# Kernel optimization log

Hardware: AMD Instinct MI355X
Metric: run time of the kernel (lower is better)

## Reference

```python
import jax, jax.numpy as jnp
import numpy as np

NUM_EMBEDDINGS = 512
EMBEDDING_DIM = 256
COMMITMENT_COST = 0.25


def setup_inputs() -> dict:
    key = jax.random.key(0)
    k1, k2 = jax.random.split(key)
    z_e = jax.random.normal(k1, (16, EMBEDDING_DIM, 16, 16, 16), dtype=jnp.float32)
    # codebook init: uniform(-1/K, 1/K) as in the torch module
    codebook = jax.random.uniform(
        k2, (NUM_EMBEDDINGS, EMBEDDING_DIM), dtype=jnp.float32,
        minval=-1.0 / NUM_EMBEDDINGS, maxval=1.0 / NUM_EMBEDDINGS)
    return {"z_e": z_e, "codebook": codebook}


def reference(z_e, codebook):
    # z_e: [B, C, D, H, W] -> [B, D, H, W, C]
    z_p = jnp.transpose(z_e, (0, 2, 3, 4, 1))
    spatial_shape = z_p.shape[:-1]
    flat = z_p.reshape(-1, EMBEDDING_DIM)                      # [N, C]
    z_sq = jnp.sum(flat * flat, axis=1, keepdims=True)         # [N, 1]
    cb_sq = jnp.sum(codebook * codebook, axis=1)[None, :]      # [1, K]
    dot = flat @ codebook.T                                    # [N, K]
    distances = z_sq + cb_sq - 2.0 * dot
    idx = jnp.argmin(distances, axis=1)                        # [N]
    z_q_p = codebook[idx].reshape(z_p.shape)                   # [B, D, H, W, C]
    codebook_loss = jnp.mean((z_q_p - jax.lax.stop_gradient(z_p)) ** 2)
    commitment_loss = jnp.mean((z_p - jax.lax.stop_gradient(z_q_p)) ** 2)
    vq_loss = codebook_loss + COMMITMENT_COST * commitment_loss
    # straight-through estimator
    z_q_st = z_p + jax.lax.stop_gradient(z_q_p - z_p)
    z_q = jnp.transpose(z_q_st, (0, 4, 1, 2, 3))               # [B, C, D, H, W]
    encoding_indices = idx.reshape(spatial_shape)
    return z_q, vq_loss, encoding_indices
```

## Files before the change

kernel.cpp:

```cpp
#include <hip/hip_runtime.h>

#define NPOS   65536
#define CDIM   256
#define KCODES 512
#define ZTOT   16777216
#define IDX_OFF (ZTOT + 1)
#define TAU    2.0e-3f
#define GL_CAP 16384

#define WS_CBSQ 64
#define WS_CBBF 66112
#define WS_GLI  132096
#define NC_FULL 0x7fff

using bf16x8 = __attribute__((ext_vector_type(8))) short;
using f32x4  = __attribute__((ext_vector_type(4))) float;

__device__ __forceinline__ unsigned short f2bf(float f) {
    unsigned int u = __float_as_uint(f);
    return (unsigned short)((u + 0x7fffu + ((u >> 16) & 1u)) >> 16);
}

__device__ __forceinline__ float np_pw128_sq(const float* a) {
    float r[8];
    #pragma unroll
    for (int j = 0; j < 8; ++j) r[j] = __fmul_rn(a[j], a[j]);
    #pragma unroll 1
    for (int i = 8; i < 128; i += 8) {
        #pragma unroll
        for (int j = 0; j < 8; ++j)
            r[j] = __fadd_rn(r[j], __fmul_rn(a[i + j], a[i + j]));
    }
    return __fadd_rn(__fadd_rn(__fadd_rn(r[0], r[1]), __fadd_rn(r[2], r[3])),
                     __fadd_rn(__fadd_rn(r[4], r[5]), __fadd_rn(r[6], r[7])));
}

__global__ void vq_cvtprep(const float* __restrict__ cb, float* __restrict__ ws) {
    const int k = blockIdx.x;
    const int c = threadIdx.x;
    __shared__ float row[256];
    __shared__ float chres[16];
    const float v = cb[(size_t)k * CDIM + c];
    row[c] = v;
    unsigned short* cbf2 = (unsigned short*)(ws + WS_CBBF);
    const int kt = c >> 5, g = (c & 31) >> 3, j = c & 7;
    cbf2[((((k >> 4) * 8 + kt) * 64) + g * 16 + (k & 15)) * 8 + j] = f2bf(v);
    if (k == 0 && c == 0) { ws[0] = 0.0f; ((int*)ws)[1] = 0; }
    __syncthreads();
    if (c < 16) {
        const float* a = &row[(c & 8) * 16];
        const int jj = c & 7;
        float r = __fmul_rn(a[jj], a[jj]);
        #pragma unroll 1
        for (int m = 1; m < 16; ++m)
            r = __fadd_rn(r, __fmul_rn(a[jj + 8 * m], a[jj + 8 * m]));
        chres[c] = r;
    }
    __syncthreads();
    if (c == 0) {
        float h0 = __fadd_rn(__fadd_rn(__fadd_rn(chres[0], chres[1]), __fadd_rn(chres[2], chres[3])),
                             __fadd_rn(__fadd_rn(chres[4], chres[5]), __fadd_rn(chres[6], chres[7])));
        float h1 = __fadd_rn(__fadd_rn(__fadd_rn(chres[8], chres[9]), __fadd_rn(chres[10], chres[11])),
                             __fadd_rn(__fadd_rn(chres[12], chres[13]), __fadd_rn(chres[14], chres[15])));
        ws[WS_CBSQ + k] = __fadd_rn(h0, h1);
    }
}

__device__ __forceinline__ void stw(unsigned short A[2][8][64][8], int nb,
                                    int c, int q, float4 v) {
    const int kt = c >> 5, gg = (c & 31) >> 3, j = c & 7;
    unsigned short* d = &A[nb][kt][gg * 16 + q * 4][j];
    d[0]  = f2bf(v.x);
    d[8]  = f2bf(v.y);
    d[16] = f2bf(v.z);
    d[24] = f2bf(v.w);
}

__launch_bounds__(512, 2)
__global__ void vq_screen(const float* __restrict__ z,
                          float* __restrict__ ws,
                          float* __restrict__ out) {
    const int t  = threadIdx.x;
    const int w  = t >> 6;
    const int l  = t & 63;
    const int g  = l >> 4;
    const int c0 = l & 15;
    int* wsi = (int*)ws;
    const unsigned short* cbf2 = (const unsigned short*)(ws + WS_CBBF);

    __shared__ unsigned short ldsA[2][8][64][8];
    __shared__ float cbsq_s[KCODES];
    __shared__ float red_v[8][16];
    __shared__ int   red_i[8][16];
    __shared__ float fv1[16];
    __shared__ int   ccnt[16];
    __shared__ int   candk[16][8];

    cbsq_s[t] = ws[WS_CBSQ + t];
    if (t < 16) ccnt[t] = 0;

    bf16x8 bfr[4][8];
    #pragma unroll
    for (int p = 0; p < 4; ++p)
        #pragma unroll
        for (int kt = 0; kt < 8; ++kt)
            bfr[p][kt] = *(const bf16x8*)(cbf2 + ((((w * 4 + p) * 8 + kt) * 64 + l) << 3));

    const int base = blockIdx.x * 256;
    const float* zB = z + (size_t)(base >> 12) * 1048576;
    const int c1 = t >> 2, q = t & 3;

    {
        const float* zb = zB + (base & 4095);
        float4 a0 = *(const float4*)(zb + (size_t)c1 * 4096 + q * 4);
        float4 a1 = *(const float4*)(zb + (size_t)(c1 + 128) * 4096 + q * 4);
        stw(ldsA, 0, c1, q, a0);
        stw(ldsA, 0, c1 + 128, q, a1);
    }
    __syncthreads();

    #pragma unroll 1
    for (int i = 0; i < 16; ++i) {
        const int buf = i & 1;
        const int m0  = base + i * 16;

        float4 p0, p1;
        if (i < 15) {
            const float* zb = zB + ((m0 + 16) & 4095);
            p0 = *(const float4*)(zb + (size_t)c1 * 4096 + q * 4);
            p1 = *(const float4*)(zb + (size_t)(c1 + 128) * 4096 + q * 4);
        }

        f32x4 acc[4];
        #pragma unroll
        for (int p = 0; p < 4; ++p) acc[p] = (f32x4){0.f, 0.f, 0.f, 0.f};

        #pragma unroll
        for (int kt = 0; kt < 8; ++kt) {
            const bf16x8 a = *(const bf16x8*)&ldsA[buf][kt][l][0];
            acc[0] = __builtin_amdgcn_mfma_f32_16x16x32_bf16(a, bfr[0][kt], acc[0], 0, 0, 0);
            acc[1] = __builtin_amdgcn_mfma_f32_16x16x32_bf16(a, bfr[1][kt], acc[1], 0, 0, 0);
            acc[2] = __builtin_amdgcn_mfma_f32_16x16x32_bf16(a, bfr[2][kt], acc[2], 0, 0, 0);
            acc[3] = __builtin_amdgcn_mfma_f32_16x16x32_bf16(a, bfr[3][kt], acc[3], 0, 0, 0);
        }

        float v1[4]; int i1[4];
        #pragma unroll
        for (int r = 0; r < 4; ++r) { v1[r] = 3.4028235e38f; i1[r] = 0; }
        #pragma unroll
        for (int p = 0; p < 4; ++p) {
            const int k = w * 64 + p * 16 + c0;
            const float cq = cbsq_s[k];
            #pragma unroll
            for (int r = 0; r < 4; ++r) {
                const float s = fmaf(-2.0f, acc[p][r], cq);
                if (s < v1[r]) { v1[r] = s; i1[r] = k; }
            }
        }
        #pragma unroll
        for (int r = 0; r < 4; ++r) {
            #pragma unroll
            for (int m = 1; m < 16; m <<= 1) {
                float pv = __shfl_xor(v1[r], m, 64);
                int   pi = __shfl_xor(i1[r], m, 64);
                if (pv < v1[r] || (pv == v1[r] && pi < i1[r])) { v1[r] = pv; i1[r] = pi; }
            }
        }
        if (c0 == 0) {
            #pragma unroll
            for (int r = 0; r < 4; ++r) {
                red_v[w][g * 4 + r] = v1[r];
                red_i[w][g * 4 + r] = i1[r];
            }
        }
        __syncthreads();

        float gv = 0.f; int gi = 0;
        if (t < 16) {
            gv = red_v[0][t]; gi = red_i[0][t];
            #pragma unroll
            for (int ww = 1; ww < 8; ++ww) {
                const float pv = red_v[ww][t];
                const int   pi = red_i[ww][t];
                if (pv < gv || (pv == gv && pi < gi)) { gv = pv; gi = pi; }
            }
            fv1[t] = gv;
        }
        __syncthreads();

        #pragma unroll
        for (int p = 0; p < 4; ++p) {
            const int k = w * 64 + p * 16 + c0;
            const float cq = cbsq_s[k];
            #pragma unroll
            for (int r = 0; r < 4; ++r) {
                const float s = fmaf(-2.0f, acc[p][r], cq);
                const int row = g * 4 + r;
                if (s < fv1[row] + TAU) {
                    int pos = atomicAdd(&ccnt[row], 1);
                    if (pos < 8) candk[row][pos] = k;
                }
            }
        }
        if (i < 15) {
            stw(ldsA, buf ^ 1, c1, q, p0);
            stw(ldsA, buf ^ 1, c1 + 128, q, p1);
        }
        __syncthreads();

        if (t < 16) {
            const int n = m0 + t;
            out[IDX_OFF + n] = (float)gi;
            const int nc = ccnt[t];
            if (nc > 1) {
                int slot = atomicAdd(wsi + 1, 1);
                if (slot < GL_CAP) {
                    int* gl = wsi + WS_GLI + slot * 10;
                    gl[0] = n;
                    gl[1] = (nc > 8) ? NC_FULL : nc;
                    #pragma unroll
                    for (int qq = 0; qq < 8; ++qq)
                        gl[2 + qq] = (qq < nc && qq < 8) ? candk[t][qq] : 0;
                }
            }
            ccnt[t] = 0;
        }
    }
}

__global__ void vq_refine(const float* __restrict__ z,
                          const float* __restrict__ cb,
                          float* __restrict__ ws,
                          float* __restrict__ out) {
    int* wsi = (int*)ws;
    const int cnt = min(wsi[1], GL_CAP);
    const int t   = threadIdx.x;
    const int wid = t >> 6;
    const int l   = t & 63;

    __shared__ __align__(16) float zs[260];
    __shared__ float chres[16];
    __shared__ float zsq_sh;
    __shared__ float wbv[4];
    __shared__ int   wbi[4];

    for (int slot = blockIdx.x; slot < cnt; slot += gridDim.x) {
        __syncthreads();
        const int* gl = wsi + WS_GLI + slot * 10;
        const int n  = gl[0];
        const int nc = gl[1];
        const size_t zb = (size_t)(n >> 12) * 1048576 + (size_t)(n & 4095);
        zs[t] = z[zb + (size_t)t * 4096];
        __syncthreads();

        if (t < 16) {
            const float* a = &zs[(t & 8) * 16];
            const int j = t & 7;
            float r = __fmul_rn(a[j], a[j]);
            #pragma unroll 1
            for (int m = 1; m < 16; ++m)
                r = __fadd_rn(r, __fmul_rn(a[j + 8 * m], a[j + 8 * m]));
            chres[t] = r;
        }
        __syncthreads();
        if (t == 0) {
            float h0 = __fadd_rn(__fadd_rn(__fadd_rn(chres[0], chres[1]), __fadd_rn(chres[2], chres[3])),
                                 __fadd_rn(__fadd_rn(chres[4], chres[5]), __fadd_rn(chres[6], chres[7])));
            float h1 = __fadd_rn(__fadd_rn(__fadd_rn(chres[8], chres[9]), __fadd_rn(chres[10], chres[11])),
                                 __fadd_rn(__fadd_rn(chres[12], chres[13]), __fadd_rn(chres[14], chres[15])));
            zsq_sh = __fadd_rn(h0, h1);
        }
        __syncthreads();
        const float zsq = zsq_sh;
        const float4 zl = *(const float4*)&zs[4 * l];

        float bv = 3.4028235e38f;
        int   bi = 0x7fffffff;
        if (nc != NC_FULL) {
            for (int ci = wid; ci < nc; ci += 4) {
                const int k = gl[2 + ci];
                const float4 e = *(const float4*)(cb + (size_t)k * CDIM + 4 * l);
                double d = (double)e.x * (double)zl.x + (double)e.y * (double)zl.y
                         + (double)e.z * (double)zl.z + (double)e.w * (double)zl.w;
                #pragma unroll
                for (int m = 1; m < 64; m <<= 1)
                    d += __shfl_xor(d, m, 64);
                const float dist = __fsub_rn(__fadd_rn(zsq, ws[WS_CBSQ + k]),
                                             __fmul_rn(2.0f, (float)d));
                if (dist < bv || (dist == bv && k < bi)) { bv = dist; bi = k; }
            }
        } else {
            for (int k = wid; k < KCODES; k += 4) {
                const float4 e = *(const float4*)(cb + (size_t)k * CDIM + 4 * l);
                double d = (double)e.x * (double)zl.x + (double)e.y * (double)zl.y
                         + (double)e.z * (double)zl.z + (double)e.w * (double)zl.w;
                #pragma unroll
                for (int m = 1; m < 64; m <<= 1)
                    d += __shfl_xor(d, m, 64);
                const float dist = __fsub_rn(__fadd_rn(zsq, ws[WS_CBSQ + k]),
                                             __fmul_rn(2.0f, (float)d));
                if (dist < bv || (dist == bv && k < bi)) { bv = dist; bi = k; }
            }
        }
        if (l == 0) { wbv[wid] = bv; wbi[wid] = bi; }
        __syncthreads();
        if (t == 0) {
            float v = wbv[0]; int i = wbi[0];
            #pragma unroll
            for (int ww = 1; ww < 4; ++ww) {
                if (wbv[ww] < v || (wbv[ww] == v && wbi[ww] < i)) { v = wbv[ww]; i = wbi[ww]; }
            }
            out[IDX_OFF + n] = (float)i;
        }
    }
}

__launch_bounds__(256, 4)
__global__ void vq_gather(const float* __restrict__ z,
                          const float* __restrict__ cb,
                          float* __restrict__ out,
                          float* __restrict__ ws) {
    __shared__ int   sidx[32];
    __shared__ float lcb[32][257];
    const int t  = threadIdx.x;
    const int n0 = blockIdx.x * 32;
    const int b  = n0 >> 12;
    const int s0 = n0 & 4095;

    if (t < 32) sidx[t] = (int)out[IDX_OFF + n0 + t];
    __syncthreads();

    #pragma unroll 4
    for (int e = t; e < 32 * 256; e += 256) {
        const int r = e >> 8, c = e & 255;
        lcb[r][c] = cb[(size_t)sidx[r] * CDIM + c];
    }
    __syncthreads();

    float acc = 0.0f;
    const int sl = t & 31, cg = t >> 5;
    const size_t base = (size_t)b * 1048576 + (size_t)s0 + sl;
    #pragma unroll 4
    for (int i = 0; i < 32; ++i) {
        const int c = i * 8 + cg;
        const size_t o = base + (size_t)c * 4096;
        float v  = lcb[sl][c];
        float zv = z[o];
        out[o] = v;
        float df = v - zv;
        acc += df * df;
    }

    #pragma unroll
    for (int off = 32; off > 0; off >>= 1)
        acc += __shfl_down(acc, off, 64);
    __shared__ float wsum[4];
    const int lane = t & 63, wid = t >> 6;
    if (lane == 0) wsum[wid] = acc;
    __syncthreads();
    if (t == 0)
        atomicAdd(&ws[0], wsum[0] + wsum[1] + wsum[2] + wsum[3]);
}

__global__ void vq_fin(const float* __restrict__ ws, float* __restrict__ out) {
    if (threadIdx.x == 0)
        out[ZTOT] = 1.25f * ws[0] / (float)ZTOT;
}

extern "C" void kernel_launch(void* const* d_in, const int* in_sizes, int n_in,
                              void* d_out, int out_size, void* d_ws, size_t ws_size,
                              hipStream_t stream) {
    const float* z  = (const float*)d_in[0];
    const float* cb = (const float*)d_in[1];
    float* out = (float*)d_out;
    float* ws  = (float*)d_ws;

    vq_cvtprep<<<512, 256, 0, stream>>>(cb, ws);
    vq_screen<<<NPOS / 256, 512, 0, stream>>>(z, ws, out);
    vq_refine<<<2048, 256, 0, stream>>>(z, cb, ws, out);
    vq_gather<<<NPOS / 32, 256, 0, stream>>>(z, cb, out, ws);
    vq_fin<<<1, 64, 0, stream>>>(ws, out);
}
```

Baseline: 166.9 us.

## Process 32 rows per iteration with warp-specialized prefetch and vectorized gather

The screening kernel now handles 32 positions per iteration as two MFMA M-tiles, so each codebook B-fragment held in registers is reused twice and the number of loop iterations and block barriers is halved. Half the threads prefetch the next tile and write it to LDS while the other half reduce the argmin. The index and candidate-list output for an iteration is deferred to the next one, which needs double-buffered candidate counters. The gather kernel switches to float4 global loads and stores. This raises register and LDS use, which may reduce occupancy.

```diff
diff --git a/kernel.cpp b/kernel.cpp
--- a/kernel.cpp
+++ b/kernel.cpp
@@ -7,6 +7,7 @@
 #define IDX_OFF (ZTOT + 1)
 #define TAU    2.0e-3f
 #define GL_CAP 16384
+#define NIT    8
 
 #define WS_CBSQ 64
 #define WS_CBBF 66112
@@ -66,10 +67,11 @@
     }
 }
 
-__device__ __forceinline__ void stw(unsigned short A[2][8][64][8], int nb,
-                                    int c, int q, float4 v) {
+__device__ __forceinline__ void stw32(unsigned short A[2][8][2][64][8], int nb,
+                                      int c, int q, float4 v) {
     const int kt = c >> 5, gg = (c & 31) >> 3, j = c & 7;
-    unsigned short* d = &A[nb][kt][gg * 16 + q * 4][j];
+    const int mt = q >> 2, lr = (q & 3) * 4;
+    unsigned short* d = &A[nb][kt][mt][gg * 16 + lr][j];
     d[0]  = f2bf(v.x);
     d[8]  = f2bf(v.y);
     d[16] = f2bf(v.z);
@@ -88,16 +90,16 @@
     int* wsi = (int*)ws;
     const unsigned short* cbf2 = (const unsigned short*)(ws + WS_CBBF);
 
-    __shared__ unsigned short ldsA[2][8][64][8];
+    __shared__ unsigned short ldsA[2][8][2][64][8];
     __shared__ float cbsq_s[KCODES];
-    __shared__ float red_v[8][16];
-    __shared__ int   red_i[8][16];
-    __shared__ float fv1[16];
-    __shared__ int   ccnt[16];
-    __shared__ int   candk[16][8];
+    __shared__ float red_v[8][32];
+    __shared__ int   red_i[8][32];
+    __shared__ float fv1[32];
+    __shared__ int   ccnt[2][32];
+    __shared__ int   candk[2][32][8];
 
     cbsq_s[t] = ws[WS_CBSQ + t];
-    if (t < 16) ccnt[t] = 0;
+    if (t < 64) ccnt[t >> 5][t & 31] = 0;
 
     bf16x8 bfr[4][8];
     #pragma unroll
@@ -106,85 +108,133 @@
         for (int kt = 0; kt < 8; ++kt)
             bfr[p][kt] = *(const bf16x8*)(cbf2 + ((((w * 4 + p) * 8 + kt) * 64 + l) << 3));
 
-    const int base = blockIdx.x * 256;
+    const int base  = blockIdx.x * 256;
+    const int sbase = base & 4095;
     const float* zB = z + (size_t)(base >> 12) * 1048576;
-    const int c1 = t >> 2, q = t & 3;
-
-    {
-        const float* zb = zB + (base & 4095);
-        float4 a0 = *(const float4*)(zb + (size_t)c1 * 4096 + q * 4);
-        float4 a1 = *(const float4*)(zb + (size_t)(c1 + 128) * 4096 + q * 4);
-        stw(ldsA, 0, c1, q, a0);
-        stw(ldsA, 0, c1 + 128, q, a1);
-    }
-    __syncthreads();
+
+    #pragma unroll
+    for (int i = 0; i < 4; ++i) {
+        const int e = t + 512 * i;
+        const int c = e >> 3, q = e & 7;
+        float4 v = *(const float4*)(zB + (size_t)c * 4096 + sbase + q * 4);
+        stw32(ldsA, 0, c, q, v);
+    }
+    __syncthreads();
+
+    int gi_prev = 0;
 
     #pragma unroll 1
-    for (int i = 0; i < 16; ++i) {
-        const int buf = i & 1;
-        const int m0  = base + i * 16;
-
-        float4 p0, p1;
-        if (i < 15) {
-            const float* zb = zB + ((m0 + 16) & 4095);
-            p0 = *(const float4*)(zb + (size_t)c1 * 4096 + q * 4);
-            p1 = *(const float4*)(zb + (size_t)(c1 + 128) * 4096 + q * 4);
-        }
-
-        f32x4 acc[4];
-        #pragma unroll
-        for (int p = 0; p < 4; ++p) acc[p] = (f32x4){0.f, 0.f, 0.f, 0.f};
-
+    for (int it = 0; it < NIT; ++it) {
+        const int buf = it & 1;
+
+        float4 pf[8];
+        if (t >= 256 && it < NIT - 1) {
+            const int sn = sbase + (it + 1) * 32;
+            #pragma unroll
+            for (int i = 0; i < 8; ++i) {
+                const int e = (t - 256) + 256 * i;
+                const int c = e >> 3, q = e & 7;
+                pf[i] = *(const float4*)(zB + (size_t)c * 4096 + sn + q * 4);
+            }
+        }
+
+        f32x4 acc[4][2];
+        #pragma unroll
+        for (int p = 0; p < 4; ++p) {
+            acc[p][0] = (f32x4){0.f, 0.f, 0.f, 0.f};
+            acc[p][1] = (f32x4){0.f, 0.f, 0.f, 0.f};
+        }
         #pragma unroll
         for (int kt = 0; kt < 8; ++kt) {
-            const bf16x8 a = *(const bf16x8*)&ldsA[buf][kt][l][0];
-            acc[0] = __builtin_amdgcn_mfma_f32_16x16x32_bf16(a, bfr[0][kt], acc[0], 0, 0, 0);
-            acc[1] = __builtin_amdgcn_mfma_f32_16x16x32_bf16(a, bfr[1][kt], acc[1], 0, 0, 0);
-            acc[2] = __builtin_amdgcn_mfma_f32_16x16x32_bf16(a, bfr[2][kt], acc[2], 0, 0, 0);
-            acc[3] = __builtin_amdgcn_mfma_f32_16x16x32_bf16(a, bfr[3][kt], acc[3], 0, 0, 0);
-        }
-
-        float v1[4]; int i1[4];
-        #pragma unroll
-        for (int r = 0; r < 4; ++r) { v1[r] = 3.4028235e38f; i1[r] = 0; }
+            const bf16x8 a0 = *(const bf16x8*)&ldsA[buf][kt][0][l][0];
+            const bf16x8 a1 = *(const bf16x8*)&ldsA[buf][kt][1][l][0];
+            #pragma unroll
+            for (int p = 0; p < 4; ++p) {
+                acc[p][0] = __builtin_amdgcn_mfma_f32_16x16x32_bf16(a0, bfr[p][kt], acc[p][0], 0, 0, 0);
+                acc[p][1] = __builtin_amdgcn_mfma_f32_16x16x32_bf16(a1, bfr[p][kt], acc[p][1], 0, 0, 0);
+            }
+        }
+
+        float v1[2][4]; int i1[2][4];
+        #pragma unroll
+        for (int mt = 0; mt < 2; ++mt)
+            #pragma unroll
+            for (int r = 0; r < 4; ++r) { v1[mt][r] = 3.4028235e38f; i1[mt][r] = 0; }
         #pragma unroll
         for (int p = 0; p < 4; ++p) {
             const int k = w * 64 + p * 16 + c0;
             const float cq = cbsq_s[k];
             #pragma unroll
+            for (int mt = 0; mt < 2; ++mt)
+                #pragma unroll
+                for (int r = 0; r < 4; ++r) {
+                    const float s = fmaf(-2.0f, acc[p][mt][r], cq);
+                    if (s < v1[mt][r]) { v1[mt][r] = s; i1[mt][r] = k; }
+                }
+        }
+        #pragma unroll
+        for (int mt = 0; mt < 2; ++mt)
+            #pragma unroll
             for (int r = 0; r < 4; ++r) {
-                const float s = fmaf(-2.0f, acc[p][r], cq);
-                if (s < v1[r]) { v1[r] = s; i1[r] = k; }
-            }
-        }
-        #pragma unroll
-        for (int r = 0; r < 4; ++r) {
-            #pragma unroll
-            for (int m = 1; m < 16; m <<= 1) {
-                float pv = __shfl_xor(v1[r], m, 64);
-                int   pi = __shfl_xor(i1[r], m, 64);
-                if (pv < v1[r] || (pv == v1[r] && pi < i1[r])) { v1[r] = pv; i1[r] = pi; }
-            }
-        }
+                #pragma unroll
+                for (int m = 1; m < 16; m <<= 1) {
+                    const float pv = __shfl_xor(v1[mt][r], m, 64);
+                    const int   pi = __shfl_xor(i1[mt][r], m, 64);
+                    if (pv < v1[mt][r] || (pv == v1[mt][r] && pi < i1[mt][r])) {
+                        v1[mt][r] = pv; i1[mt][r] = pi;
+                    }
+                }
+            }
         if (c0 == 0) {
             #pragma unroll
-            for (int r = 0; r < 4; ++r) {
-                red_v[w][g * 4 + r] = v1[r];
-                red_i[w][g * 4 + r] = i1[r];
-            }
-        }
-        __syncthreads();
-
-        float gv = 0.f; int gi = 0;
-        if (t < 16) {
-            gv = red_v[0][t]; gi = red_i[0][t];
-            #pragma unroll
-            for (int ww = 1; ww < 8; ++ww) {
-                const float pv = red_v[ww][t];
-                const int   pi = red_i[ww][t];
-                if (pv < gv || (pv == gv && pi < gi)) { gv = pv; gi = pi; }
-            }
-            fv1[t] = gv;
+            for (int mt = 0; mt < 2; ++mt)
+                #pragma unroll
+                for (int r = 0; r < 4; ++r) {
+                    red_v[w][mt * 16 + g * 4 + r] = v1[mt][r];
+                    red_i[w][mt * 16 + g * 4 + r] = i1[mt][r];
+                }
+        }
+        __syncthreads();
+
+        if (t < 256) {
+            const int row = t >> 3, ww = t & 7;
+            float mv = red_v[ww][row];
+            int   mi = red_i[ww][row];
+            #pragma unroll
+            for (int d = 1; d < 8; d <<= 1) {
+                const float ov = __shfl_xor(mv, d, 64);
+                const int   oi = __shfl_xor(mi, d, 64);
+                if (ov < mv || (ov == mv && oi < mi)) { mv = ov; mi = oi; }
+            }
+            if (ww == 0) {
+                fv1[row] = mv;
+                if (it > 0) {
+                    const int pp = (it - 1) & 1;
+                    const int np = base + (it - 1) * 32 + row;
+                    out[IDX_OFF + np] = (float)gi_prev;
+                    const int nc = ccnt[pp][row];
+                    if (nc > 1) {
+                        int slot = atomicAdd(wsi + 1, 1);
+                        if (slot < GL_CAP) {
+                            int* gl = wsi + WS_GLI + slot * 10;
+                            gl[0] = np;
+                            gl[1] = (nc > 8) ? NC_FULL : nc;
+                            #pragma unroll
+                            for (int q = 0; q < 8; ++q)
+                                gl[2 + q] = (q < nc && q < 8) ? candk[pp][row][q] : 0;
+                        }
+                    }
+                    ccnt[pp][row] = 0;
+                }
+                gi_prev = mi;
+            }
+        } else if (it < NIT - 1) {
+            #pragma unroll
+            for (int i = 0; i < 8; ++i) {
+                const int e = (t - 256) + 256 * i;
+                const int c = e >> 3, q = e & 7;
+                stw32(ldsA, buf ^ 1, c, q, pf[i]);
+            }
         }
         __syncthreads();
 
@@ -193,37 +243,36 @@
             const int k = w * 64 + p * 16 + c0;
             const float cq = cbsq_s[k];
             #pragma unroll
-            for (int r = 0; r < 4; ++r) {
-                const float s = fmaf(-2.0f, acc[p][r], cq);
-                const int row = g * 4 + r;
-                if (s < fv1[row] + TAU) {
-                    int pos = atomicAdd(&ccnt[row], 1);
-                    if (pos < 8) candk[row][pos] = k;
+            for (int mt = 0; mt < 2; ++mt)
+                #pragma unroll
+                for (int r = 0; r < 4; ++r) {
+                    const float s = fmaf(-2.0f, acc[p][mt][r], cq);
+                    const int row = mt * 16 + g * 4 + r;
+                    if (s < fv1[row] + TAU) {
+                        int pos = atomicAdd(&ccnt[buf][row], 1);
+                        if (pos < 8) candk[buf][row][pos] = k;
+                    }
                 }
-            }
-        }
-        if (i < 15) {
-            stw(ldsA, buf ^ 1, c1, q, p0);
-            stw(ldsA, buf ^ 1, c1 + 128, q, p1);
-        }
-        __syncthreads();
-
-        if (t < 16) {
-            const int n = m0 + t;
-            out[IDX_OFF + n] = (float)gi;
-            const int nc = ccnt[t];
-            if (nc > 1) {
-                int slot = atomicAdd(wsi + 1, 1);
-                if (slot < GL_CAP) {
-                    int* gl = wsi + WS_GLI + slot * 10;
-                    gl[0] = n;
-                    gl[1] = (nc > 8) ? NC_FULL : nc;
-                    #pragma unroll
-                    for (int qq = 0; qq < 8; ++qq)
-                        gl[2 + qq] = (qq < nc && qq < 8) ? candk[t][qq] : 0;
-                }
-            }
-            ccnt[t] = 0;
+        }
+    }
+
+    __syncthreads();
+    if (t < 256 && (t & 7) == 0) {
+        const int row = t >> 3;
+        const int pp = (NIT - 1) & 1;
+        const int np = base + (NIT - 1) * 32 + row;
+        out[IDX_OFF + np] = (float)gi_prev;
+        const int nc = ccnt[pp][row];
+        if (nc > 1) {
+            int slot = atomicAdd(wsi + 1, 1);
+            if (slot < GL_CAP) {
+                int* gl = wsi + WS_GLI + slot * 10;
+                gl[0] = np;
+                gl[1] = (nc > 8) ? NC_FULL : nc;
+                #pragma unroll
+                for (int q = 0; q < 8; ++q)
+                    gl[2 + q] = (q < nc && q < 8) ? candk[pp][row][q] : 0;
+            }
         }
     }
 }
@@ -338,17 +387,22 @@
     __syncthreads();
 
     float acc = 0.0f;
-    const int sl = t & 31, cg = t >> 5;
-    const size_t base = (size_t)b * 1048576 + (size_t)s0 + sl;
-    #pragma unroll 4
-    for (int i = 0; i < 32; ++i) {
-        const int c = i * 8 + cg;
-        const size_t o = base + (size_t)c * 4096;
-        float v  = lcb[sl][c];
-        float zv = z[o];
-        out[o] = v;
-        float df = v - zv;
-        acc += df * df;
+    const int pq = t & 7, ch0 = t >> 3;
+    const size_t zbase = (size_t)b * 1048576 + (size_t)s0;
+    #pragma unroll
+    for (int pass = 0; pass < 8; ++pass) {
+        const int c = pass * 32 + ch0;
+        const size_t o = zbase + (size_t)c * 4096 + pq * 4;
+        const float4 zv = *(const float4*)(z + o);
+        float4 v;
+        v.x = lcb[pq * 4 + 0][c];
+        v.y = lcb[pq * 4 + 1][c];
+        v.z = lcb[pq * 4 + 2][c];
+        v.w = lcb[pq * 4 + 3][c];
+        *(float4*)(out + o) = v;
+        const float dx = v.x - zv.x, dy = v.y - zv.y;
+        const float dz = v.z - zv.z, dw = v.w - zv.w;
+        acc += dx * dx + dy * dy + dz * dz + dw * dw;
     }
 
     #pragma unroll
```

After: 187.8 us. 1.13x slower.
